# Optimization experiments

Measured on AMD Instinct MI355X. Metric: run time of the kernel, lower is better.

The kernel has to match this reference:

```python
import jax, jax.numpy as jnp
import numpy as np
import math

EMBED_DIM = 1024
N_HEADS = 16
HEAD_DIM = EMBED_DIM // N_HEADS


def setup_inputs() -> dict:
    key = jax.random.key(0)
    k1, k2, k3, k4 = jax.random.split(key, 4)
    B, S, D = 2, 2048, EMBED_DIM
    inputs = jax.random.normal(k1, (B, S, D), dtype=jnp.float32)
    cross_embeddings = jax.random.normal(k2, (B, S, D), dtype=jnp.float32)
    # learned params
    ln_weight = jnp.ones((D,), dtype=jnp.float32)
    ln_bias = jnp.zeros((D,), dtype=jnp.float32)
    # nn.Linear weights are [out_features, in_features]
    kv_weight = jax.random.normal(k3, (2 * D, D), dtype=jnp.float32) * (1.0 / math.sqrt(D))
    q_weight = jax.random.normal(k4, (D, D), dtype=jnp.float32) * (1.0 / math.sqrt(D))
    return {
        "inputs": inputs,
        "cross_embeddings": cross_embeddings,
        "ln_weight": ln_weight,
        "ln_bias": ln_bias,
        "kv_weight": kv_weight,
        "q_weight": q_weight,
    }


def _layer_norm(x, w, b, eps=1e-5):
    mu = jnp.mean(x, axis=-1, keepdims=True)
    var = jnp.mean(jnp.square(x - mu), axis=-1, keepdims=True)
    return (x - mu) * jax.lax.rsqrt(var + eps) * w + b


def reference(inputs, cross_embeddings, ln_weight, ln_bias, kv_weight, q_weight):
    B, S, D = inputs.shape
    H, Dh = N_HEADS, HEAD_DIM
    resid = inputs
    x = _layer_norm(inputs, ln_weight, ln_bias)
    # kv projection on cross embeddings: y = x @ W^T
    kv = jnp.einsum('bsd,ed->bse', cross_embeddings, kv_weight)  # [B,S,2D]
    k, v = kv[..., :D], kv[..., D:]
    q = jnp.einsum('bsd,ed->bse', x, q_weight)  # [B,S,D]
    q = q.reshape(B, S, H, Dh).transpose(0, 2, 1, 3)  # [B,H,S,Dh]
    k = k.reshape(B, S, H, Dh).transpose(0, 2, 1, 3)
    v = v.reshape(B, S, H, Dh).transpose(0, 2, 1, 3)
    attn = jnp.einsum('bhqd,bhkd->bhqk', q, k) / math.sqrt(Dh)
    attn = jax.nn.softmax(attn, axis=-1)
    out = jnp.einsum('bhqk,bhkd->bhqd', attn, v)  # [B,H,S,Dh]
    out = out.transpose(0, 2, 1, 3).reshape(B, S, D)
    return out + resid
```

## Files before the change

kernel.cpp:

```cpp
#include <hip/hip_runtime.h>
#include <cstdint>
#include <cstddef>


typedef float  f32x4  __attribute__((ext_vector_type(4)));
typedef __bf16 bf16x8 __attribute__((ext_vector_type(8)));
typedef __bf16 bf16x4 __attribute__((ext_vector_type(4)));
typedef __bf16 bf16x2 __attribute__((ext_vector_type(2)));

#define MFMA16(a, b, c) __builtin_amdgcn_mfma_f32_16x16x32_bf16((a), (b), (c), 0, 0, 0)

__device__ __forceinline__ void gll16(const void* g, void* l) {
  __builtin_amdgcn_global_load_lds(
      (const __attribute__((address_space(1))) unsigned int*)g,
      (__attribute__((address_space(3))) unsigned int*)l, 16, 0, 0);
}

__device__ __forceinline__ bf16x2 split2(float x) {
  bf16x2 r;
  __bf16 hh = (__bf16)x;
  r[0] = hh;
  r[1] = (__bf16)(x - (float)hh);
  return r;
}

__global__ __launch_bounds__(256) void prep_kernel(
    const float* __restrict__ x, const float* __restrict__ w, const float* __restrict__ b,
    __bf16* __restrict__ xh, __bf16* __restrict__ xl,
    const float* __restrict__ c,  __bf16* __restrict__ ch, __bf16* __restrict__ cl,
    const float* __restrict__ kw, __bf16* __restrict__ kh, __bf16* __restrict__ kl,
    const float* __restrict__ qw, __bf16* __restrict__ qh, __bf16* __restrict__ ql)
{
  const int tid = threadIdx.x;
  if (blockIdx.x < 4096) {
    const int row = blockIdx.x;
    const float4 v = *reinterpret_cast<const float4*>(x + (size_t)row * 1024 + tid * 4);
    float s  = v.x + v.y + v.z + v.w;
    float s2 = v.x * v.x + v.y * v.y + v.z * v.z + v.w * v.w;
#pragma unroll
    for (int o = 1; o < 64; o <<= 1) { s += __shfl_xor(s, o, 64); s2 += __shfl_xor(s2, o, 64); }
    __shared__ float red[8];
    const int wv = tid >> 6, ln = tid & 63;
    if (ln == 0) { red[wv] = s; red[4 + wv] = s2; }
    __syncthreads();
    s  = red[0] + red[1] + red[2] + red[3];
    s2 = red[4] + red[5] + red[6] + red[7];
    const float mu = s * (1.f / 1024.f);
    const float rs = rsqrtf(s2 * (1.f / 1024.f) - mu * mu + 1e-5f);
    const float4 wv4 = *reinterpret_cast<const float4*>(w + tid * 4);
    const float4 bv4 = *reinterpret_cast<const float4*>(b + tid * 4);
    float o4[4] = {(v.x - mu) * rs * wv4.x + bv4.x, (v.y - mu) * rs * wv4.y + bv4.y,
                   (v.z - mu) * rs * wv4.z + bv4.z, (v.w - mu) * rs * wv4.w + bv4.w};
    bf16x4 h, l;
#pragma unroll
    for (int i = 0; i < 4; ++i) { bf16x2 hl = split2(o4[i]); h[i] = hl[0]; l[i] = hl[1]; }
    *reinterpret_cast<bf16x4*>(xh + (size_t)row * 1024 + tid * 4) = h;
    *reinterpret_cast<bf16x4*>(xl + (size_t)row * 1024 + tid * 4) = l;
  } else {
    const int i = ((blockIdx.x - 4096) * 256 + tid) * 4;
    const float* src; __bf16 *dh, *dl; int off;
    if (i < 4194304)      { src = c;  dh = ch; dl = cl; off = i; }
    else if (i < 6291456) { src = kw; dh = kh; dl = kl; off = i - 4194304; }
    else                  { src = qw; dh = qh; dl = ql; off = i - 6291456; }
    const float4 v = *reinterpret_cast<const float4*>(src + off);
    float o4[4] = {v.x, v.y, v.z, v.w};
    bf16x4 h, l;
#pragma unroll
    for (int j = 0; j < 4; ++j) { bf16x2 hl = split2(o4[j]); h[j] = hl[0]; l[j] = hl[1]; }
    *reinterpret_cast<bf16x4*>(dh + off) = h;
    *reinterpret_cast<bf16x4*>(dl + off) = l;
  }
}

__device__ __forceinline__ void gemm_tile(
    const __bf16* __restrict__ Ah, const __bf16* __restrict__ Al,
    const __bf16* __restrict__ Bh, const __bf16* __restrict__ Bl,
    __bf16* __restrict__ C, int N, int m0, int n0, char* ldsb)
{
  constexpr int K = 1024;
  const int tid  = threadIdx.x;
  const int wave = tid >> 6, lane = tid & 63;
  const int g = lane >> 4, qm = lane & 15;
  const int wr = wave >> 1, wc = wave & 1;

  f32x4 acc[4][4] = {};

  const int rr = tid >> 2;
  const int cc = tid & 3;
  const int wb = wave * 1024;

  for (int k0 = 0; k0 < K; k0 += 32) {
    const size_t a0 = (size_t)(m0 + rr) * K + k0 + cc * 8;
    const size_t a1 = (size_t)(m0 + 64 + rr) * K + k0 + cc * 8;
    const size_t b0 = (size_t)(n0 + rr) * K + k0 + cc * 8;
    const size_t b1 = (size_t)(n0 + 64 + rr) * K + k0 + cc * 8;
    gll16(Ah + a0, ldsb + 0     + wb);
    gll16(Ah + a1, ldsb + 4096  + wb);
    gll16(Al + a0, ldsb + 8192  + wb);
    gll16(Al + a1, ldsb + 12288 + wb);
    gll16(Bh + b0, ldsb + 16384 + wb);
    gll16(Bh + b1, ldsb + 20480 + wb);
    gll16(Bl + b0, ldsb + 24576 + wb);
    gll16(Bl + b1, ldsb + 28672 + wb);
    __syncthreads();

    bf16x8 bhf[4], blf[4];
#pragma unroll
    for (int nt = 0; nt < 4; ++nt) {
      const int brow = wc * 64 + nt * 16 + qm;
      const char* bp = ldsb + 16384 + brow * 64 + g * 16;
      bhf[nt] = *reinterpret_cast<const bf16x8*>(bp);
      blf[nt] = *reinterpret_cast<const bf16x8*>(bp + 8192);
    }
#pragma unroll
    for (int mt = 0; mt < 4; ++mt) {
      const int arow = wr * 64 + mt * 16 + qm;
      const char* ap = ldsb + arow * 64 + g * 16;
      const bf16x8 ahf = *reinterpret_cast<const bf16x8*>(ap);
      const bf16x8 alf = *reinterpret_cast<const bf16x8*>(ap + 8192);
#pragma unroll
      for (int nt = 0; nt < 4; ++nt) {
        acc[mt][nt] = MFMA16(ahf, bhf[nt], acc[mt][nt]);
        acc[mt][nt] = MFMA16(ahf, blf[nt], acc[mt][nt]);
        acc[mt][nt] = MFMA16(alf, bhf[nt], acc[mt][nt]);
      }
    }
    __syncthreads();
  }

#pragma unroll
  for (int mt = 0; mt < 4; ++mt)
#pragma unroll
    for (int nt = 0; nt < 4; ++nt) {
      const int col = n0 + wc * 64 + nt * 16 + qm;
#pragma unroll
      for (int r = 0; r < 4; ++r) {
        const int row = m0 + wr * 64 + mt * 16 + g * 4 + r;
        C[(size_t)row * N + col] = (__bf16)acc[mt][nt][r];
      }
    }
}

__global__ __launch_bounds__(256) void gemm2_kernel(
    const __bf16* __restrict__ cAh, const __bf16* __restrict__ cAl,
    const __bf16* __restrict__ kWh, const __bf16* __restrict__ kWl, __bf16* __restrict__ kvC,
    const __bf16* __restrict__ xAh, const __bf16* __restrict__ xAl,
    const __bf16* __restrict__ qWh, const __bf16* __restrict__ qWl, __bf16* __restrict__ qC)
{
  __shared__ __bf16 lds[4 * 128 * 32];
  int t = blockIdx.x;
  if (t < 512)
    gemm_tile(cAh, cAl, kWh, kWl, kvC, 2048, (t >> 4) * 128, (t & 15) * 128, (char*)lds);
  else {
    t -= 512;
    gemm_tile(xAh, xAl, qWh, qWl, qC, 1024, (t >> 3) * 128, (t & 7) * 128, (char*)lds);
  }
}

__global__ __launch_bounds__(256) void gemm1_kernel(
    const __bf16* __restrict__ Ah, const __bf16* __restrict__ Al,
    const __bf16* __restrict__ Bh, const __bf16* __restrict__ Bl,
    __bf16* __restrict__ C, int N)
{
  __shared__ __bf16 lds[4 * 128 * 32];
  gemm_tile(Ah, Al, Bh, Bl, C, N, blockIdx.y * 128, blockIdx.x * 128, (char*)lds);
}

__global__ __launch_bounds__(512) void attn_kernel(
    const __bf16* __restrict__ qb, const __bf16* __restrict__ kvb,
    const float* __restrict__ resid, float* __restrict__ out)
{
  const int bh = blockIdx.y, b = bh >> 4, h = bh & 15;
  const int q0 = blockIdx.x * 128;
  const int tid = threadIdx.x, wave = tid >> 6, lane = tid & 63;
  const int g = lane >> 4, qm = lane & 15;

  __shared__ __bf16 Kl[2][64 * 64];
  __shared__ __bf16 Vt[2][64 * 64];
  __shared__ __bf16 Pl[8][16 * 80];

  bf16x8 qf[2];
  {
    const size_t row = (size_t)(b * 2048 + q0 + wave * 16 + qm);
    const __bf16* p = qb + row * 1024 + h * 64 + g * 8;
    qf[0] = *reinterpret_cast<const bf16x8*>(p);
    qf[1] = *reinterpret_cast<const bf16x8*>(p + 32);
  }

  float lsum[4] = {0.f, 0.f, 0.f, 0.f};
  f32x4 acco[4] = {};
  const float scale2 = 0.125f * 1.44269504f;

  const int krow  = wave * 8 + (lane >> 3);
  const int kchnk = (lane & 7) ^ (krow & 7);
  const int vd0 = wave * 8;

  const size_t kv_base = (size_t)(b * 2048) * 2048 + h * 64;

  gll16(kvb + kv_base + (size_t)krow * 2048 + kchnk * 8, (char*)Kl[0] + wave * 1024);
  bf16x8 vreg = *reinterpret_cast<const bf16x8*>(
      kvb + kv_base + (size_t)lane * 2048 + 1024 + vd0);
  {
#pragma unroll
    for (int j = 0; j < 8; ++j) {
      const int d = vd0 + j;
      const int ch = (lane >> 3) ^ (d & 7);
      Vt[0][d * 64 + ch * 8 + (lane & 7)] = vreg[j];
    }
  }
  __syncthreads();

  for (int t = 0; t < 32; ++t) {
    const int cur = t & 1, nxt = cur ^ 1;
    if (t < 31) {
      const size_t key0 = (size_t)(t + 1) * 64;
      gll16(kvb + kv_base + (key0 + krow) * 2048 + kchnk * 8,
            (char*)Kl[nxt] + wave * 1024);
      vreg = *reinterpret_cast<const bf16x8*>(
          kvb + kv_base + (key0 + lane) * 2048 + 1024 + vd0);
    }

    f32x4 s[4] = {};
    __builtin_amdgcn_s_setprio(1);
#pragma unroll
    for (int kt = 0; kt < 4; ++kt) {
      const int row = kt * 16 + qm;
#pragma unroll
      for (int kk = 0; kk < 2; ++kk) {
        const int ch = (kk * 4 + g) ^ (qm & 7);
        const bf16x8 kf = *reinterpret_cast<const bf16x8*>(&Kl[cur][row * 64 + ch * 8]);
        s[kt] = MFMA16(qf[kk], kf, s[kt]);
      }
    }
    __builtin_amdgcn_s_setprio(0);

#pragma unroll
    for (int r = 0; r < 4; ++r) {
#pragma unroll
      for (int kt = 0; kt < 4; ++kt) {
        const float p = exp2f(s[kt][r] * scale2);
        lsum[r] += p;
        Pl[wave][(g * 4 + r) * 80 + kt * 16 + qm] = (__bf16)p;
      }
    }

    __builtin_amdgcn_s_setprio(1);
#pragma unroll
    for (int ks = 0; ks < 2; ++ks) {
      const bf16x8 pf = *reinterpret_cast<const bf16x8*>(&Pl[wave][qm * 80 + ks * 32 + g * 8]);
#pragma unroll
      for (int dt = 0; dt < 4; ++dt) {
        const int drow = dt * 16 + qm;
        const int ch = (ks * 4 + g) ^ (qm & 7);
        const bf16x8 vf = *reinterpret_cast<const bf16x8*>(&Vt[cur][drow * 64 + ch * 8]);
        acco[dt] = MFMA16(pf, vf, acco[dt]);
      }
    }
    __builtin_amdgcn_s_setprio(0);

    if (t < 31) {
#pragma unroll
      for (int j = 0; j < 8; ++j) {
        const int d = vd0 + j;
        const int ch = (lane >> 3) ^ (d & 7);
        Vt[nxt][d * 64 + ch * 8 + (lane & 7)] = vreg[j];
      }
    }
    __syncthreads();
  }

#pragma unroll
  for (int r = 0; r < 4; ++r) {
#pragma unroll
    for (int o = 1; o < 16; o <<= 1) lsum[r] += __shfl_xor(lsum[r], o, 64);
  }
#pragma unroll
  for (int dt = 0; dt < 4; ++dt) {
    const int col = h * 64 + dt * 16 + qm;
#pragma unroll
    for (int r = 0; r < 4; ++r) {
      const size_t tok = (size_t)(b * 2048 + q0 + wave * 16 + g * 4 + r);
      out[tok * 1024 + col] = acco[dt][r] / lsum[r] + resid[tok * 1024 + col];
    }
  }
}

extern "C" void kernel_launch(void* const* d_in, const int* in_sizes, int n_in,
                              void* d_out, int out_size, void* d_ws, size_t ws_size,
                              hipStream_t stream)
{
  const float* inputs = (const float*)d_in[0];
  const float* cross  = (const float*)d_in[1];
  const float* lnw    = (const float*)d_in[2];
  const float* lnb    = (const float*)d_in[3];
  const float* kvw    = (const float*)d_in[4];
  const float* qw     = (const float*)d_in[5];
  float* out = (float*)d_out;

  char* ws = (char*)d_ws;
  const size_t MB = (size_t)1 << 20;
  __bf16* xh  = (__bf16*)(ws + 0 * MB);
  __bf16* xl  = (__bf16*)(ws + 8 * MB);
  __bf16* chh = (__bf16*)(ws + 16 * MB);
  __bf16* cll = (__bf16*)(ws + 24 * MB);
  __bf16* kwh = (__bf16*)(ws + 32 * MB);
  __bf16* kwl = (__bf16*)(ws + 36 * MB);
  __bf16* qwh = (__bf16*)(ws + 40 * MB);
  __bf16* qwl = (__bf16*)(ws + 42 * MB);
  __bf16* kvb = (__bf16*)(ws + 44 * MB);
  const bool merged = ws_size >= 68 * MB;
  __bf16* qbb = merged ? (__bf16*)(ws + 60 * MB) : (__bf16*)(ws + 16 * MB);

  prep_kernel<<<11264, 256, 0, stream>>>(inputs, lnw, lnb, xh, xl,
                                         cross, chh, cll, kvw, kwh, kwl, qw, qwh, qwl);
  if (merged) {
    gemm2_kernel<<<768, 256, 0, stream>>>(chh, cll, kwh, kwl, kvb,
                                          xh, xl, qwh, qwl, qbb);
  } else {
    gemm1_kernel<<<dim3(16, 32), 256, 0, stream>>>(chh, cll, kwh, kwl, kvb, 2048);
    gemm1_kernel<<<dim3(8, 32), 256, 0, stream>>>(xh, xl, qwh, qwl, qbb, 1024);
  }
  attn_kernel<<<dim3(16, 32), 512, 0, stream>>>(qbb, kvb, inputs, out);
}
```

Before: 247.9 us.

## Fold softmax scale into Q projection and restructure prep kernel grid

The layer-norm part of the prep kernel now handles one row per wave with a pure shuffle reduction, so the shared-memory sync is gone. The conversion part becomes a grid-stride loop over 1024 blocks instead of 7168 small blocks. The softmax scale and log2e factor are multiplied into the Q GEMM epilogue, which removes a multiply per score in the attention inner loop. The P staging row stride also shrinks from 80 to 72, which changes the LDS bank pattern. Scaling Q before rounding to bf16 slightly changes numerics.

```diff
diff --git a/kernel.cpp b/kernel.cpp
--- a/kernel.cpp
+++ b/kernel.cpp
@@ -32,50 +32,59 @@
     const float* __restrict__ qw, __bf16* __restrict__ qh, __bf16* __restrict__ ql)
 {
   const int tid = threadIdx.x;
-  if (blockIdx.x < 4096) {
-    const int row = blockIdx.x;
-    const float4 v = *reinterpret_cast<const float4*>(x + (size_t)row * 1024 + tid * 4);
-    float s  = v.x + v.y + v.z + v.w;
-    float s2 = v.x * v.x + v.y * v.y + v.z * v.z + v.w * v.w;
+  if (blockIdx.x < 1024) {
+    const int wave = tid >> 6, lane = tid & 63;
+    const int row = blockIdx.x * 4 + wave;
+    const float* xr = x + (size_t)row * 1024;
+    float4 v[4];
+#pragma unroll
+    for (int j = 0; j < 4; ++j)
+      v[j] = *reinterpret_cast<const float4*>(xr + j * 256 + lane * 4);
+    float s = 0.f, s2 = 0.f;
+#pragma unroll
+    for (int j = 0; j < 4; ++j) {
+      s  += v[j].x + v[j].y + v[j].z + v[j].w;
+      s2 += v[j].x * v[j].x + v[j].y * v[j].y + v[j].z * v[j].z + v[j].w * v[j].w;
+    }
 #pragma unroll
     for (int o = 1; o < 64; o <<= 1) { s += __shfl_xor(s, o, 64); s2 += __shfl_xor(s2, o, 64); }
-    __shared__ float red[8];
-    const int wv = tid >> 6, ln = tid & 63;
-    if (ln == 0) { red[wv] = s; red[4 + wv] = s2; }
-    __syncthreads();
-    s  = red[0] + red[1] + red[2] + red[3];
-    s2 = red[4] + red[5] + red[6] + red[7];
     const float mu = s * (1.f / 1024.f);
     const float rs = rsqrtf(s2 * (1.f / 1024.f) - mu * mu + 1e-5f);
-    const float4 wv4 = *reinterpret_cast<const float4*>(w + tid * 4);
-    const float4 bv4 = *reinterpret_cast<const float4*>(b + tid * 4);
-    float o4[4] = {(v.x - mu) * rs * wv4.x + bv4.x, (v.y - mu) * rs * wv4.y + bv4.y,
-                   (v.z - mu) * rs * wv4.z + bv4.z, (v.w - mu) * rs * wv4.w + bv4.w};
-    bf16x4 h, l;
-#pragma unroll
-    for (int i = 0; i < 4; ++i) { bf16x2 hl = split2(o4[i]); h[i] = hl[0]; l[i] = hl[1]; }
-    *reinterpret_cast<bf16x4*>(xh + (size_t)row * 1024 + tid * 4) = h;
-    *reinterpret_cast<bf16x4*>(xl + (size_t)row * 1024 + tid * 4) = l;
+#pragma unroll
+    for (int j = 0; j < 4; ++j) {
+      const float4 wv = *reinterpret_cast<const float4*>(w + j * 256 + lane * 4);
+      const float4 bv = *reinterpret_cast<const float4*>(b + j * 256 + lane * 4);
+      float o4[4] = {(v[j].x - mu) * rs * wv.x + bv.x, (v[j].y - mu) * rs * wv.y + bv.y,
+                     (v[j].z - mu) * rs * wv.z + bv.z, (v[j].w - mu) * rs * wv.w + bv.w};
+      bf16x4 h, l;
+#pragma unroll
+      for (int i = 0; i < 4; ++i) { bf16x2 hl = split2(o4[i]); h[i] = hl[0]; l[i] = hl[1]; }
+      *reinterpret_cast<bf16x4*>(xh + (size_t)row * 1024 + j * 256 + lane * 4) = h;
+      *reinterpret_cast<bf16x4*>(xl + (size_t)row * 1024 + j * 256 + lane * 4) = l;
+    }
   } else {
-    const int i = ((blockIdx.x - 4096) * 256 + tid) * 4;
-    const float* src; __bf16 *dh, *dl; int off;
-    if (i < 4194304)      { src = c;  dh = ch; dl = cl; off = i; }
-    else if (i < 6291456) { src = kw; dh = kh; dl = kl; off = i - 4194304; }
-    else                  { src = qw; dh = qh; dl = ql; off = i - 6291456; }
-    const float4 v = *reinterpret_cast<const float4*>(src + off);
-    float o4[4] = {v.x, v.y, v.z, v.w};
-    bf16x4 h, l;
-#pragma unroll
-    for (int j = 0; j < 4; ++j) { bf16x2 hl = split2(o4[j]); h[j] = hl[0]; l[j] = hl[1]; }
-    *reinterpret_cast<bf16x4*>(dh + off) = h;
-    *reinterpret_cast<bf16x4*>(dl + off) = l;
+    size_t i4 = (size_t)(blockIdx.x - 1024) * 256 + tid;
+#pragma unroll
+    for (int it = 0; it < 7; ++it, i4 += 262144) {
+      const float* src; __bf16 *dh, *dl; size_t off4;
+      if (i4 < 1048576)      { src = c;  dh = ch; dl = cl; off4 = i4; }
+      else if (i4 < 1572864) { src = kw; dh = kh; dl = kl; off4 = i4 - 1048576; }
+      else                   { src = qw; dh = qh; dl = ql; off4 = i4 - 1572864; }
+      const float4 v = reinterpret_cast<const float4*>(src)[off4];
+      float o4[4] = {v.x, v.y, v.z, v.w};
+      bf16x4 h, l;
+#pragma unroll
+      for (int j = 0; j < 4; ++j) { bf16x2 hl = split2(o4[j]); h[j] = hl[0]; l[j] = hl[1]; }
+      reinterpret_cast<bf16x4*>(dh)[off4] = h;
+      reinterpret_cast<bf16x4*>(dl)[off4] = l;
+    }
   }
 }
 
 __device__ __forceinline__ void gemm_tile(
     const __bf16* __restrict__ Ah, const __bf16* __restrict__ Al,
     const __bf16* __restrict__ Bh, const __bf16* __restrict__ Bl,
-    __bf16* __restrict__ C, int N, int m0, int n0, char* ldsb)
+    __bf16* __restrict__ C, int N, int m0, int n0, char* ldsb, float cscale)
 {
   constexpr int K = 1024;
   const int tid  = threadIdx.x;
@@ -136,10 +145,12 @@
 #pragma unroll
       for (int r = 0; r < 4; ++r) {
         const int row = m0 + wr * 64 + mt * 16 + g * 4 + r;
-        C[(size_t)row * N + col] = (__bf16)acc[mt][nt][r];
-      }
-    }
-}
+        C[(size_t)row * N + col] = (__bf16)(acc[mt][nt][r] * cscale);
+      }
+    }
+}
+
+#define QSCALE (0.125f * 1.44269504f)
 
 __global__ __launch_bounds__(256) void gemm2_kernel(
     const __bf16* __restrict__ cAh, const __bf16* __restrict__ cAl,
@@ -150,20 +161,20 @@
   __shared__ __bf16 lds[4 * 128 * 32];
   int t = blockIdx.x;
   if (t < 512)
-    gemm_tile(cAh, cAl, kWh, kWl, kvC, 2048, (t >> 4) * 128, (t & 15) * 128, (char*)lds);
+    gemm_tile(cAh, cAl, kWh, kWl, kvC, 2048, (t >> 4) * 128, (t & 15) * 128, (char*)lds, 1.0f);
   else {
     t -= 512;
-    gemm_tile(xAh, xAl, qWh, qWl, qC, 1024, (t >> 3) * 128, (t & 7) * 128, (char*)lds);
+    gemm_tile(xAh, xAl, qWh, qWl, qC, 1024, (t >> 3) * 128, (t & 7) * 128, (char*)lds, QSCALE);
   }
 }
 
 __global__ __launch_bounds__(256) void gemm1_kernel(
     const __bf16* __restrict__ Ah, const __bf16* __restrict__ Al,
     const __bf16* __restrict__ Bh, const __bf16* __restrict__ Bl,
-    __bf16* __restrict__ C, int N)
+    __bf16* __restrict__ C, int N, float cscale)
 {
   __shared__ __bf16 lds[4 * 128 * 32];
-  gemm_tile(Ah, Al, Bh, Bl, C, N, blockIdx.y * 128, blockIdx.x * 128, (char*)lds);
+  gemm_tile(Ah, Al, Bh, Bl, C, N, blockIdx.y * 128, blockIdx.x * 128, (char*)lds, cscale);
 }
 
 __global__ __launch_bounds__(512) void attn_kernel(
@@ -177,7 +188,7 @@
 
   __shared__ __bf16 Kl[2][64 * 64];
   __shared__ __bf16 Vt[2][64 * 64];
-  __shared__ __bf16 Pl[8][16 * 80];
+  __shared__ __bf16 Pl[8][16 * 72];
 
   bf16x8 qf[2];
   {
@@ -189,7 +200,6 @@
 
   float lsum[4] = {0.f, 0.f, 0.f, 0.f};
   f32x4 acco[4] = {};
-  const float scale2 = 0.125f * 1.44269504f;
 
   const int krow  = wave * 8 + (lane >> 3);
   const int kchnk = (lane & 7) ^ (krow & 7);
@@ -238,16 +248,16 @@
     for (int r = 0; r < 4; ++r) {
 #pragma unroll
       for (int kt = 0; kt < 4; ++kt) {
-        const float p = exp2f(s[kt][r] * scale2);
+        const float p = exp2f(s[kt][r]);
         lsum[r] += p;
-        Pl[wave][(g * 4 + r) * 80 + kt * 16 + qm] = (__bf16)p;
+        Pl[wave][(g * 4 + r) * 72 + kt * 16 + qm] = (__bf16)p;
       }
     }
 
     __builtin_amdgcn_s_setprio(1);
 #pragma unroll
     for (int ks = 0; ks < 2; ++ks) {
-      const bf16x8 pf = *reinterpret_cast<const bf16x8*>(&Pl[wave][qm * 80 + ks * 32 + g * 8]);
+      const bf16x8 pf = *reinterpret_cast<const bf16x8*>(&Pl[wave][qm * 72 + ks * 32 + g * 8]);
 #pragma unroll
       for (int dt = 0; dt < 4; ++dt) {
         const int drow = dt * 16 + qm;
@@ -311,14 +321,14 @@
   const bool merged = ws_size >= 68 * MB;
   __bf16* qbb = merged ? (__bf16*)(ws + 60 * MB) : (__bf16*)(ws + 16 * MB);
 
-  prep_kernel<<<11264, 256, 0, stream>>>(inputs, lnw, lnb, xh, xl,
-                                         cross, chh, cll, kvw, kwh, kwl, qw, qwh, qwl);
+  prep_kernel<<<2048, 256, 0, stream>>>(inputs, lnw, lnb, xh, xl,
+                                        cross, chh, cll, kvw, kwh, kwl, qw, qwh, qwl);
   if (merged) {
     gemm2_kernel<<<768, 256, 0, stream>>>(chh, cll, kwh, kwl, kvb,
                                           xh, xl, qwh, qwl, qbb);
   } else {
-    gemm1_kernel<<<dim3(16, 32), 256, 0, stream>>>(chh, cll, kwh, kwl, kvb, 2048);
-    gemm1_kernel<<<dim3(8, 32), 256, 0, stream>>>(xh, xl, qwh, qwl, qbb, 1024);
+    gemm1_kernel<<<dim3(16, 32), 256, 0, stream>>>(chh, cll, kwh, kwl, kvb, 2048, 1.0f);
+    gemm1_kernel<<<dim3(8, 32), 256, 0, stream>>>(xh, xl, qwh, qwl, qbb, 1024, QSCALE);
   }
   attn_kernel<<<dim3(16, 32), 512, 0, stream>>>(qbb, kvb, inputs, out);
 }
```

New measurement: 266.4 us. 7.5% more time.
